# Optimization experiments

Hardware: AMD Instinct MI355X
Metric: run time of the kernel (lower is better)

## Reference

```python
import jax, jax.numpy as jnp
import numpy as np

EPS = 1e-6

def rmsnorm(x, weight):
    # reduce over last dim d
    inv = jax.lax.rsqrt(jnp.mean(x * x, axis=-1, keepdims=True) + EPS)
    return x * inv * weight

def setup_inputs() -> dict:
    key = jax.random.key(0)
    k1, k2 = jax.random.split(key)
    L, B, T, D = 8, 4, 4096, 1024
    blocks = jax.random.normal(k1, (L, B, T, D), dtype=jnp.float32)
    query = jax.random.normal(k2, (D,), dtype=jnp.float32)
    norm_weight = jnp.ones((D,), dtype=jnp.float32)
    return {"blocks": blocks, "query": query, "norm_weight": norm_weight}

def reference(blocks, query, norm_weight):
    # blocks == V: [l, b, t, d] stacked block representations
    V = blocks
    K = rmsnorm(V, norm_weight)                      # [l,b,t,d]
    logits = jnp.einsum('d,lbtd->lbt', query, K)     # [l,b,t]
    attn = jax.nn.softmax(logits, axis=0)            # softmax over block axis l
    h = jnp.einsum('lbt,lbtd->btd', attn, V)         # [b,t,d]
    return h
```

## Files before the change

### kernel.cpp

```cpp
#include <hip/hip_runtime.h>
#include <math.h>


#define LL   8
#define DD   1024
#define TPB  256
#define EPSF 1e-6f

__global__ __launch_bounds__(TPB) void block_attn_kernel(
    const float* __restrict__ blocks,
    const float* __restrict__ query,
    const float* __restrict__ norm_weight,
    float* __restrict__ out,
    size_t l_stride)
{
    const int bt  = blockIdx.x;
    const int tid = threadIdx.x;
    const int d0  = tid * 4;

    const float4 q = *reinterpret_cast<const float4*>(query + d0);
    const float4 w = *reinterpret_cast<const float4*>(norm_weight + d0);
    const float qw0 = q.x * w.x, qw1 = q.y * w.y, qw2 = q.z * w.z, qw3 = q.w * w.w;

    const float* base = blocks + (size_t)bt * DD + d0;

    float4 v[LL];
    float  ss[LL];
    float  qd[LL];
#pragma unroll
    for (int l = 0; l < LL; ++l) {
        v[l]  = *reinterpret_cast<const float4*>(base + (size_t)l * l_stride);
        ss[l] = v[l].x * v[l].x + v[l].y * v[l].y + v[l].z * v[l].z + v[l].w * v[l].w;
        qd[l] = qw0 * v[l].x + qw1 * v[l].y + qw2 * v[l].z + qw3 * v[l].w;
    }

#pragma unroll
    for (int l = 0; l < LL; ++l) {
#pragma unroll
        for (int off = 32; off > 0; off >>= 1) {
            ss[l] += __shfl_down(ss[l], off, 64);
            qd[l] += __shfl_down(qd[l], off, 64);
        }
    }

    __shared__ float red[4][LL][2];
    const int wave = tid >> 6;
    const int lane = tid & 63;
    if (lane == 0) {
#pragma unroll
        for (int l = 0; l < LL; ++l) {
            red[wave][l][0] = ss[l];
            red[wave][l][1] = qd[l];
        }
    }
    __syncthreads();

    __shared__ float attn_s[LL];
    if (tid == 0) {
        float logits[LL];
        float m = -INFINITY;
#pragma unroll
        for (int l = 0; l < LL; ++l) {
            const float s  = red[0][l][0] + red[1][l][0] + red[2][l][0] + red[3][l][0];
            const float qq = red[0][l][1] + red[1][l][1] + red[2][l][1] + red[3][l][1];
            const float lg = qq * rsqrtf(s * (1.0f / DD) + EPSF);
            logits[l] = lg;
            m = fmaxf(m, lg);
        }
        float sum = 0.f;
        float e[LL];
#pragma unroll
        for (int l = 0; l < LL; ++l) { e[l] = expf(logits[l] - m); sum += e[l]; }
        const float inv = 1.0f / sum;
#pragma unroll
        for (int l = 0; l < LL; ++l) attn_s[l] = e[l] * inv;
    }
    __syncthreads();

    float4 h = make_float4(0.f, 0.f, 0.f, 0.f);
#pragma unroll
    for (int l = 0; l < LL; ++l) {
        const float a = attn_s[l];
        h.x += a * v[l].x;
        h.y += a * v[l].y;
        h.z += a * v[l].z;
        h.w += a * v[l].w;
    }
    *reinterpret_cast<float4*>(out + (size_t)bt * DD + d0) = h;
}

extern "C" void kernel_launch(void* const* d_in, const int* in_sizes, int n_in,
                              void* d_out, int out_size, void* d_ws, size_t ws_size,
                              hipStream_t stream) {
    const float* blocks      = (const float*)d_in[0];
    const float* query       = (const float*)d_in[1];
    const float* norm_weight = (const float*)d_in[2];
    float*       out         = (float*)d_out;

    const size_t l_stride = (size_t)out_size;
    const int    n_bt     = out_size / DD;

    block_attn_kernel<<<n_bt, TPB, 0, stream>>>(blocks, query, norm_weight, out, l_stride);
}
```

Measured before the change: 118.9 us.

## Use butterfly transpose-reduction for 16 sums and nontemporal loads/stores

Replaces 16 independent 6-step shuffle reductions with a recursive-halving butterfly that reduces all 16 partial sums (8 sum-of-squares, 8 query dots) together, cutting shuffle count from 96 to about 17 per thread. The final softmax is now spread across 8 lanes with shuffles instead of running serially in thread 0. Block loads and output stores use nontemporal hints to avoid polluting cache for streamed data. The kernel is memory-bound, so the reduction savings may be hidden behind memory traffic.

```diff
diff --git a/kernel.cpp b/kernel.cpp
--- a/kernel.cpp
+++ b/kernel.cpp
@@ -7,6 +7,8 @@
 #define TPB  256
 #define EPSF 1e-6f
 
+typedef float fx4 __attribute__((ext_vector_type(4)));
+
 __global__ __launch_bounds__(TPB) void block_attn_kernel(
     const float* __restrict__ blocks,
     const float* __restrict__ query,
@@ -14,70 +16,95 @@
     float* __restrict__ out,
     size_t l_stride)
 {
-    const int bt  = blockIdx.x;
-    const int tid = threadIdx.x;
-    const int d0  = tid * 4;
+    const int bt   = blockIdx.x;
+    const int tid  = threadIdx.x;
+    const int lane = tid & 63;
+    const int wave = tid >> 6;
+    const int d0   = tid * 4;
 
-    const float4 q = *reinterpret_cast<const float4*>(query + d0);
-    const float4 w = *reinterpret_cast<const float4*>(norm_weight + d0);
+    const fx4 q = *reinterpret_cast<const fx4*>(query + d0);
+    const fx4 w = *reinterpret_cast<const fx4*>(norm_weight + d0);
     const float qw0 = q.x * w.x, qw1 = q.y * w.y, qw2 = q.z * w.z, qw3 = q.w * w.w;
 
     const float* base = blocks + (size_t)bt * DD + d0;
 
-    float4 v[LL];
-    float  ss[LL];
-    float  qd[LL];
+    fx4   v[LL];
+    float x[16];
 #pragma unroll
     for (int l = 0; l < LL; ++l) {
-        v[l]  = *reinterpret_cast<const float4*>(base + (size_t)l * l_stride);
-        ss[l] = v[l].x * v[l].x + v[l].y * v[l].y + v[l].z * v[l].z + v[l].w * v[l].w;
-        qd[l] = qw0 * v[l].x + qw1 * v[l].y + qw2 * v[l].z + qw3 * v[l].w;
+        v[l] = __builtin_nontemporal_load(
+                 reinterpret_cast<const fx4*>(base + (size_t)l * l_stride));
+    }
+#pragma unroll
+    for (int l = 0; l < LL; ++l) {
+        x[l]     = v[l].x * v[l].x + v[l].y * v[l].y + v[l].z * v[l].z + v[l].w * v[l].w;
+        x[8 + l] = qw0 * v[l].x + qw1 * v[l].y + qw2 * v[l].z + qw3 * v[l].w;
     }
 
+    float y[8];
+    {
+        const bool b = lane & 1;
 #pragma unroll
-    for (int l = 0; l < LL; ++l) {
-#pragma unroll
-        for (int off = 32; off > 0; off >>= 1) {
-            ss[l] += __shfl_down(ss[l], off, 64);
-            qd[l] += __shfl_down(qd[l], off, 64);
+        for (int k = 0; k < 8; ++k) {
+            const float mine = b ? x[2*k + 1] : x[2*k];
+            const float oth  = b ? x[2*k]     : x[2*k + 1];
+            y[k] = mine + __shfl_xor(oth, 1);
         }
     }
+    float z[4];
+    {
+        const bool b = lane & 2;
+#pragma unroll
+        for (int j = 0; j < 4; ++j) {
+            const float mine = b ? y[2*j + 1] : y[2*j];
+            const float oth  = b ? y[2*j]     : y[2*j + 1];
+            z[j] = mine + __shfl_xor(oth, 2);
+        }
+    }
+    float t2[2];
+    {
+        const bool b = lane & 4;
+#pragma unroll
+        for (int i = 0; i < 2; ++i) {
+            const float mine = b ? z[2*i + 1] : z[2*i];
+            const float oth  = b ? z[2*i]     : z[2*i + 1];
+            t2[i] = mine + __shfl_xor(oth, 4);
+        }
+    }
+    float u;
+    {
+        const bool b = lane & 8;
+        const float mine = b ? t2[1] : t2[0];
+        const float oth  = b ? t2[0] : t2[1];
+        u = mine + __shfl_xor(oth, 8);
+    }
+    u += __shfl_xor(u, 16);
+    u += __shfl_xor(u, 32);
 
-    __shared__ float red[4][LL][2];
-    const int wave = tid >> 6;
-    const int lane = tid & 63;
-    if (lane == 0) {
-#pragma unroll
-        for (int l = 0; l < LL; ++l) {
-            red[wave][l][0] = ss[l];
-            red[wave][l][1] = qd[l];
-        }
+    __shared__ float red[4][16];
+    if (lane < 16) red[wave][lane] = u;
+    __syncthreads();
+
+    __shared__ float attn_s[LL];
+    if (tid < 8) {
+        const int l = tid;
+        const float s  = red[0][l]     + red[1][l]     + red[2][l]     + red[3][l];
+        const float qq = red[0][l + 8] + red[1][l + 8] + red[2][l + 8] + red[3][l + 8];
+        const float lg = qq * rsqrtf(s * (1.0f / DD) + EPSF);
+        float m = lg;
+        m = fmaxf(m, __shfl_xor(m, 1));
+        m = fmaxf(m, __shfl_xor(m, 2));
+        m = fmaxf(m, __shfl_xor(m, 4));
+        const float e = expf(lg - m);
+        float ssum = e;
+        ssum += __shfl_xor(ssum, 1);
+        ssum += __shfl_xor(ssum, 2);
+        ssum += __shfl_xor(ssum, 4);
+        attn_s[l] = e / ssum;
     }
     __syncthreads();
 
-    __shared__ float attn_s[LL];
-    if (tid == 0) {
-        float logits[LL];
-        float m = -INFINITY;
-#pragma unroll
-        for (int l = 0; l < LL; ++l) {
-            const float s  = red[0][l][0] + red[1][l][0] + red[2][l][0] + red[3][l][0];
-            const float qq = red[0][l][1] + red[1][l][1] + red[2][l][1] + red[3][l][1];
-            const float lg = qq * rsqrtf(s * (1.0f / DD) + EPSF);
-            logits[l] = lg;
-            m = fmaxf(m, lg);
-        }
-        float sum = 0.f;
-        float e[LL];
-#pragma unroll
-        for (int l = 0; l < LL; ++l) { e[l] = expf(logits[l] - m); sum += e[l]; }
-        const float inv = 1.0f / sum;
-#pragma unroll
-        for (int l = 0; l < LL; ++l) attn_s[l] = e[l] * inv;
-    }
-    __syncthreads();
-
-    float4 h = make_float4(0.f, 0.f, 0.f, 0.f);
+    fx4 h = (fx4)(0.f);
 #pragma unroll
     for (int l = 0; l < LL; ++l) {
         const float a = attn_s[l];
@@ -86,7 +113,7 @@
         h.z += a * v[l].z;
         h.w += a * v[l].w;
     }
-    *reinterpret_cast<float4*>(out + (size_t)bt * DD + d0) = h;
+    __builtin_nontemporal_store(h, reinterpret_cast<fx4*>(out + (size_t)bt * DD + d0));
 }
 
 extern "C" void kernel_launch(void* const* d_in, const int* in_sizes, int n_in,
```

Result: faster. 99.87 us (-16.0%).
